# Optimization experiments

Measured on AMD Instinct MI355X. Metric: run time of the kernel, lower is better.

## Reference

```python
import jax, jax.numpy as jnp
import numpy as np

INSIZE = 512
OUTSIZE = 512
N_U = 64
N_V = 64
SIGMA_MIN = 0.1
SIGMA_MAX = 1.0
BATCH = 8192


def setup_inputs() -> dict:
    key = jax.random.key(0)
    kx, kp, ku, kv, kb = jax.random.split(key, 5)
    x = jax.random.normal(kx, (BATCH, INSIZE), dtype=jnp.float32)
    nsigma = min(INSIZE, OUTSIZE)
    p = 0.001 * jax.random.normal(kp, (nsigma,), dtype=jnp.float32)
    U = jnp.triu(jax.random.normal(ku, (INSIZE, INSIZE), dtype=jnp.float32))
    V = jnp.triu(jax.random.normal(kv, (OUTSIZE, OUTSIZE), dtype=jnp.float32))
    bound = 1.0 / float(np.sqrt(INSIZE))
    bias = jax.random.uniform(kb, (1, OUTSIZE), minval=-bound, maxval=bound, dtype=jnp.float32)
    return {"x": x, "p": p, "U": U, "V": V, "bias": bias}


def _house_chain(x, rows):
    # Sequentially apply Householder reflections. rows[i] has its leading
    # entries zeroed (upper-triangular structure), which makes the full-width
    # dot/outer-product exactly equal to torch's Hprod on the trailing slice
    # u[-k:] while leaving the leading columns of x untouched.
    def step(x, u):
        alpha = 2.0 * (x @ u) / jnp.dot(u, u)  # [B]
        return x - alpha[:, None] * u[None, :], None
    x, _ = jax.lax.scan(step, x, rows)
    return x


def _sigma_matrix(p, dtype):
    r = (SIGMA_MAX - SIGMA_MIN) / 2.0
    sigma_mean = SIGMA_MIN + r
    sigmas = 2.0 * r * (jax.nn.sigmoid(p) - 0.5) + sigma_mean  # [nsigma]
    nsigma = min(INSIZE, OUTSIZE)
    idx = jnp.arange(nsigma)
    return jnp.zeros((INSIZE, OUTSIZE), dtype=dtype).at[idx, idx].set(sigmas.astype(dtype))


def reference(x, p, U, V, bias):
    # Umultiply: i = 0 .. N_U-1, reflector U[i] with k = insize - i
    x = _house_chain(x, jnp.triu(U)[:N_U])
    # x @ Sigma (rectangular diagonal of constrained singular values)
    x = x @ _sigma_matrix(p, x.dtype)
    # Vmultiply: i = N_V-1 down to 0, reflector V[i] with k = outsize - i
    x = _house_chain(x, jnp.triu(V)[:N_V][::-1])
    return x + bias
```

## Files before the change

kernel.cpp:

```cpp
#include <hip/hip_runtime.h>
#include <hip/hip_bf16.h>
#include <math.h>


#define INSIZE 512
#define NREF 64
#define BATCH 8192

static constexpr int OFF_WT    = 0;
static constexpr int OFF_SIGMA = 131072;
static constexpr int OFF_BETAU = OFF_SIGMA + 512;
static constexpr int OFF_BETAV = OFF_BETAU + 64;
static constexpr int OFF_GU    = OFF_BETAV + 64;
static constexpr int OFF_GV    = OFF_GU + 4096;
static constexpr int OFF_C     = OFF_GV + 4096;

__device__ inline float sigma_of(float pv) {
    float s = 1.0f / (1.0f + expf(-pv));
    return 0.55f + 0.9f * (s - 0.5f);
}

__global__ __launch_bounds__(256) void k_prep(const float* __restrict__ U,
                                              const float* __restrict__ V,
                                              const float* __restrict__ p,
                                              float* __restrict__ ws) {
    int b = blockIdx.x, t = threadIdx.x;
    if (b == 192) {
        for (int c = t; c < INSIZE; c += 256)
            (ws + OFF_SIGMA)[c] = sigma_of(p[c]);
        return;
    }
    __shared__ float rowi[INSIZE];
    int w = t >> 6, l = t & 63;
    if (b < 128) {
        bool isV = (b >= 64);
        int i = isV ? (b - 64) : b;
        const float* src = isV ? V : U;
        int srow = isV ? (63 - i) : i;
        for (int c = t; c < INSIZE; c += 256) rowi[c] = src[srow * INSIZE + c];
        __syncthreads();
        float* G = ws + (isV ? OFF_GV : OFF_GU);
        float* beta = ws + (isV ? OFF_BETAV : OFF_BETAU);
        for (int jj = 0; jj < 16; ++jj) {
            int j = w * 16 + jj;
            int jrow = isV ? (63 - j) : j;
            const float* rj = src + jrow * INSIZE;
            float s = 0.f;
            for (int c = l; c < INSIZE; c += 64) s += rowi[c] * rj[c];
            for (int o = 32; o > 0; o >>= 1) s += __shfl_down(s, o, 64);
            if (l == 0) {
                G[i * 64 + j] = s;
                if (j == i) beta[i] = 2.0f / s;
            }
        }
    } else {
        int i = b - 128;
        for (int c = t; c < INSIZE; c += 256)
            rowi[c] = U[i * INSIZE + c] * sigma_of(p[c]);
        __syncthreads();
        float* C = ws + OFF_C;
        for (int jj = 0; jj < 16; ++jj) {
            int j = w * 16 + jj;
            const float* rj = V + (63 - j) * INSIZE;
            float s = 0.f;
            for (int c = l; c < INSIZE; c += 64) s += rowi[c] * rj[c];
            for (int o = 32; o > 0; o >>= 1) s += __shfl_down(s, o, 64);
            if (l == 0) C[i * 64 + j] = s;
        }
    }
}

__global__ __launch_bounds__(256) void k_WtE(const float* __restrict__ U,
                                             const float* __restrict__ V,
                                             float* __restrict__ ws) {
    __shared__ float Ps[128][34];
    __shared__ float Qs[128][34];
    __shared__ float Xs[4160];
    int t = threadIdx.x;
    int r0 = (blockIdx.x >> 4) * 32;
    int c0 = (blockIdx.x & 15) * 32;
    const float* sig = ws + OFF_SIGMA;
    float* Qf = &Qs[0][0];

    for (int i = t; i < 1024; i += 256) {
        *(float4*)&Xs[i * 4] = *(const float4*)&(ws + OFF_GU)[i * 4];
        *(float4*)&Qf[i * 4] = *(const float4*)&(ws + OFF_GV)[i * 4];
    }
    if (t < 64) {
        Xs[4096 + t] = (ws + OFF_BETAU)[t];
        Qf[4096 + t] = (ws + OFF_BETAV)[t];
    }
    __syncthreads();

    float partR[64];
    if (t < 32) {
        int r = r0 + t;
        float part[64];
#pragma unroll
        for (int j = 0; j < 64; ++j) part[j] = U[j * INSIZE + r];
#pragma unroll
        for (int m = 0; m < 64; ++m) {
            float am = part[m] * Xs[4096 + m];
            part[m] = am;
#pragma unroll
            for (int j = m + 1; j < 64; ++j)
                part[j] -= am * Xs[m * 64 + j];
        }
#pragma unroll
        for (int j = 0; j < 64; ++j) Ps[j][t] = part[j];
    } else if (t < 64) {
        int c = c0 + (t - 32);
#pragma unroll
        for (int i = 0; i < 64; ++i) partR[i] = V[(63 - i) * INSIZE + c];
#pragma unroll
        for (int i = 63; i >= 0; --i) {
            float s = partR[i];
#pragma unroll
            for (int m = i + 1; m < 64; ++m)
                s -= Qf[i * 64 + m] * partR[m];
            partR[i] = s * Qf[4096 + i];
        }
    }
    __syncthreads();

    for (int i = t; i < 1024; i += 256)
        *(float4*)&Xs[i * 4] = *(const float4*)&(ws + OFF_C)[i * 4];
    int lr = t & 31, kb = t >> 5;
    float sc = sig[c0 + lr];
#pragma unroll
    for (int ii = 0; ii < 8; ++ii) {
        int k = kb + ii * 8;
        Qs[k][lr] = U[k * INSIZE + c0 + lr] * sc;
    }
    if (t >= 32 && t < 64) {
#pragma unroll
        for (int i = 0; i < 64; ++i) Qs[64 + i][t - 32] = partR[i];
    }
    __syncthreads();

    float sr = sig[r0 + lr];
#pragma unroll
    for (int ii = 0; ii < 8; ++ii) {
        int j = kb * 8 + ii;
        float e = sr * V[(63 - j) * INSIZE + r0 + lr];
#pragma unroll 8
        for (int i = 0; i < 64; ++i)
            e -= Ps[i][lr] * Xs[i * 64 + j];
        Ps[64 + j][lr] = e;
    }
    __syncthreads();

    int ty = t >> 4, tx = t & 15;
    float a00 = 0.f, a01 = 0.f, a10 = 0.f, a11 = 0.f;
#pragma unroll
    for (int k = 0; k < 128; ++k) {
        float2 a = *(const float2*)&Ps[k][ty * 2];
        float2 bq = *(const float2*)&Qs[k][tx * 2];
        a00 += a.x * bq.x; a01 += a.x * bq.y;
        a10 += a.y * bq.x; a11 += a.y * bq.y;
    }
    int rg = r0 + ty * 2, cg = c0 + tx * 2;
    float w00 = ((rg == cg) ? sig[rg] : 0.f) - a00;
    float w01 = ((rg == cg + 1) ? sig[rg] : 0.f) - a01;
    float w10 = ((rg + 1 == cg) ? sig[rg + 1] : 0.f) - a10;
    float w11 = ((rg + 1 == cg + 1) ? sig[rg + 1] : 0.f) - a11;
    unsigned short* Wt = (unsigned short*)(ws + OFF_WT);
    __hip_bfloat162 lo = __float22bfloat162_rn(make_float2(w00, w10));
    __hip_bfloat162 hi = __float22bfloat162_rn(make_float2(w01, w11));
    *(__hip_bfloat162*)&Wt[cg * INSIZE + rg] = lo;
    *(__hip_bfloat162*)&Wt[(cg + 1) * INSIZE + rg] = hi;
}

typedef __attribute__((ext_vector_type(8))) short short8;
typedef __attribute__((ext_vector_type(4))) float float4v;

__global__ __launch_bounds__(256) void k_gemm(const float* __restrict__ X,
                                              const float* __restrict__ ws,
                                              const float* __restrict__ bias,
                                              float* __restrict__ out) {
    __shared__ float As[64 * 32];
    __shared__ unsigned short Bs[128 * 32];
    const unsigned short* Wt = (const unsigned short*)(ws + OFF_WT);

    int L = blockIdx.x;
    int inner = L & 7;
    int bn = (L >> 3) & 3;
    int bm = (L >> 5) * 8 + inner;
    int row0 = bm * 64, col0 = bn * 128;

    int t = threadIdx.x;
    int l = t & 63, w = t >> 6;
    int wm = (w & 1) * 32, wn = (w >> 1) * 64;

    float4v acc[2][4] = {};
    int quad = l >> 4;
    int lan = l & 15;

    for (int k0 = 0; k0 < INSIZE; k0 += 32) {
        __syncthreads();
#pragma unroll
        for (int i = 0; i < 2; ++i) {
            int P = i * 256 + t;
            int prow = P >> 3, pc = P & 7;
            int lc = pc ^ (prow & 7);
            const float* g = X + (size_t)(row0 + prow) * INSIZE + k0 + lc * 4;
            __builtin_amdgcn_global_load_lds(
                (const __attribute__((address_space(1))) void*)g,
                (__attribute__((address_space(3))) void*)(As + P * 4), 16, 0, 0);
        }
#pragma unroll
        for (int i = 0; i < 2; ++i) {
            int P = i * 256 + t;
            int prow = P >> 2, pc = P & 3;
            int lc = pc ^ ((prow >> 1) & 3);
            const unsigned short* g = Wt + (size_t)(col0 + prow) * INSIZE + k0 + lc * 8;
            __builtin_amdgcn_global_load_lds(
                (const __attribute__((address_space(1))) void*)g,
                (__attribute__((address_space(3))) void*)(Bs + P * 8), 16, 0, 0);
        }
        __syncthreads();

        short8 af[2];
        short8 bf[4];
#pragma unroll
        for (int mi = 0; mi < 2; ++mi) {
            int rl = wm + mi * 16 + lan;
            int c0q = quad * 2;
            const float4v lo = *(const float4v*)(As + (rl * 8 + (c0q ^ (rl & 7))) * 4);
            const float4v hi = *(const float4v*)(As + (rl * 8 + ((c0q + 1) ^ (rl & 7))) * 4);
            union { short8 s; __hip_bfloat162 h[4]; } u;
            u.h[0] = __float22bfloat162_rn(make_float2(lo[0], lo[1]));
            u.h[1] = __float22bfloat162_rn(make_float2(lo[2], lo[3]));
            u.h[2] = __float22bfloat162_rn(make_float2(hi[0], hi[1]));
            u.h[3] = __float22bfloat162_rn(make_float2(hi[2], hi[3]));
            af[mi] = u.s;
        }
#pragma unroll
        for (int ni = 0; ni < 4; ++ni) {
            int rn = wn + ni * 16 + lan;
            int c = quad ^ ((rn >> 1) & 3);
            bf[ni] = *(const short8*)(Bs + (rn * 4 + c) * 8);
        }
#pragma unroll
        for (int mi = 0; mi < 2; ++mi)
#pragma unroll
            for (int ni = 0; ni < 4; ++ni)
                acc[mi][ni] = __builtin_amdgcn_mfma_f32_16x16x32_bf16(
                    af[mi], bf[ni], acc[mi][ni], 0, 0, 0);
    }

#pragma unroll
    for (int ni = 0; ni < 4; ++ni) {
        int c = col0 + wn + ni * 16 + lan;
        float bv = bias[c];
#pragma unroll
        for (int mi = 0; mi < 2; ++mi) {
            int rbase = row0 + wm + mi * 16 + quad * 4;
#pragma unroll
            for (int r = 0; r < 4; ++r)
                out[(size_t)(rbase + r) * INSIZE + c] = acc[mi][ni][r] + bv;
        }
    }
}

extern "C" void kernel_launch(void* const* d_in, const int* in_sizes, int n_in,
                              void* d_out, int out_size, void* d_ws, size_t ws_size,
                              hipStream_t stream) {
    const float* x    = (const float*)d_in[0];
    const float* p    = (const float*)d_in[1];
    const float* U    = (const float*)d_in[2];
    const float* V    = (const float*)d_in[3];
    const float* bias = (const float*)d_in[4];
    float* ws  = (float*)d_ws;
    float* out = (float*)d_out;

    k_prep<<<193, 256, 0, stream>>>(U, V, p, ws);
    k_WtE<<<256, 256, 0, stream>>>(U, V, ws);
    k_gemm<<<512, 256, 0, stream>>>(x, ws, bias, out);
}
```

Measured before the change: 131.8 us.

## Parallelize triangular solves across full block and shrink GEMM column tile

The serial 64-step triangular solves in k_WtE, which previously ran on only 32 or 64 threads, are now spread over all 256 threads. Each lane holds 8 entries and broadcasts the pivot coefficient with a wavefront shuffle. The Gram matrices are masked to their strict triangle so the full-width update loops stay correct. The GEMM column tile also drops from 128 to 64 with twice as many blocks, raising occupancy at the cost of more redundant loading of X.

```diff
diff --git a/kernel.cpp b/kernel.cpp
--- a/kernel.cpp
+++ b/kernel.cpp
@@ -49,7 +49,8 @@
             for (int c = l; c < INSIZE; c += 64) s += rowi[c] * rj[c];
             for (int o = 32; o > 0; o >>= 1) s += __shfl_down(s, o, 64);
             if (l == 0) {
-                G[i * 64 + j] = s;
+                bool keep = isV ? (j < i) : (j > i);
+                G[i * 64 + j] = keep ? s : 0.0f;
                 if (j == i) beta[i] = 2.0f / s;
             }
         }
@@ -92,33 +93,40 @@
     }
     __syncthreads();
 
-    float partR[64];
-    if (t < 32) {
-        int r = r0 + t;
-        float part[64];
-#pragma unroll
-        for (int j = 0; j < 64; ++j) part[j] = U[j * INSIZE + r];
+    int l = t & 63;
+    int c_loc = (t >> 6) * 8 + (l >> 3);
+    int grp = l & 7;
+    int srcbase = l & 0x38;
+    float pj[8], pr[8];
+    {
+        int r = r0 + c_loc;
+#pragma unroll
+        for (int jj = 0; jj < 8; ++jj) pj[jj] = U[(grp * 8 + jj) * INSIZE + r];
 #pragma unroll
         for (int m = 0; m < 64; ++m) {
-            float am = part[m] * Xs[4096 + m];
-            part[m] = am;
-#pragma unroll
-            for (int j = m + 1; j < 64; ++j)
-                part[j] -= am * Xs[m * 64 + j];
-        }
-#pragma unroll
-        for (int j = 0; j < 64; ++j) Ps[j][t] = part[j];
-    } else if (t < 64) {
-        int c = c0 + (t - 32);
-#pragma unroll
-        for (int i = 0; i < 64; ++i) partR[i] = V[(63 - i) * INSIZE + c];
+            float tmp = pj[m & 7] * Xs[4096 + m];
+            float am = __shfl(tmp, srcbase | (m >> 3), 64);
+            if (grp == (m >> 3)) pj[m & 7] = am;
+#pragma unroll
+            for (int jj = 0; jj < 8; ++jj)
+                pj[jj] -= am * Xs[m * 64 + grp * 8 + jj];
+        }
+#pragma unroll
+        for (int jj = 0; jj < 8; ++jj) Ps[grp * 8 + jj][c_loc] = pj[jj];
+    }
+    {
+        int c = c0 + c_loc;
+#pragma unroll
+        for (int ii = 0; ii < 8; ++ii)
+            pr[ii] = V[(63 - (grp * 8 + ii)) * INSIZE + c];
 #pragma unroll
         for (int i = 63; i >= 0; --i) {
-            float s = partR[i];
-#pragma unroll
-            for (int m = i + 1; m < 64; ++m)
-                s -= Qf[i * 64 + m] * partR[m];
-            partR[i] = s * Qf[4096 + i];
+            float tmp = pr[i & 7] * Qf[4096 + i];
+            float ai = __shfl(tmp, srcbase | (i >> 3), 64);
+            if (grp == (i >> 3)) pr[i & 7] = ai;
+#pragma unroll
+            for (int ii = 0; ii < 8; ++ii)
+                pr[ii] -= ai * Qf[i * 64 + grp * 8 + ii];
         }
     }
     __syncthreads();
@@ -132,10 +140,9 @@
         int k = kb + ii * 8;
         Qs[k][lr] = U[k * INSIZE + c0 + lr] * sc;
     }
-    if (t >= 32 && t < 64) {
-#pragma unroll
-        for (int i = 0; i < 64; ++i) Qs[64 + i][t - 32] = partR[i];
-    }
+#pragma unroll
+    for (int ii = 0; ii < 8; ++ii)
+        Qs[64 + grp * 8 + ii][c_loc] = pr[ii];
     __syncthreads();
 
     float sr = sig[r0 + lr];
@@ -179,20 +186,20 @@
                                               const float* __restrict__ bias,
                                               float* __restrict__ out) {
     __shared__ float As[64 * 32];
-    __shared__ unsigned short Bs[128 * 32];
+    __shared__ unsigned short Bs[64 * 32];
     const unsigned short* Wt = (const unsigned short*)(ws + OFF_WT);
 
     int L = blockIdx.x;
     int inner = L & 7;
-    int bn = (L >> 3) & 3;
-    int bm = (L >> 5) * 8 + inner;
-    int row0 = bm * 64, col0 = bn * 128;
+    int bn = (L >> 3) & 7;
+    int bm = (L >> 6) * 8 + inner;
+    int row0 = bm * 64, col0 = bn * 64;
 
     int t = threadIdx.x;
     int l = t & 63, w = t >> 6;
-    int wm = (w & 1) * 32, wn = (w >> 1) * 64;
-
-    float4v acc[2][4] = {};
+    int wm = (w & 1) * 32, wn = (w >> 1) * 32;
+
+    float4v acc[2][2] = {};
     int quad = l >> 4;
     int lan = l & 15;
 
@@ -208,9 +215,8 @@
                 (const __attribute__((address_space(1))) void*)g,
                 (__attribute__((address_space(3))) void*)(As + P * 4), 16, 0, 0);
         }
-#pragma unroll
-        for (int i = 0; i < 2; ++i) {
-            int P = i * 256 + t;
+        {
+            int P = t;
             int prow = P >> 2, pc = P & 3;
             int lc = pc ^ ((prow >> 1) & 3);
             const unsigned short* g = Wt + (size_t)(col0 + prow) * INSIZE + k0 + lc * 8;
@@ -221,7 +227,7 @@
         __syncthreads();
 
         short8 af[2];
-        short8 bf[4];
+        short8 bf[2];
 #pragma unroll
         for (int mi = 0; mi < 2; ++mi) {
             int rl = wm + mi * 16 + lan;
@@ -236,7 +242,7 @@
             af[mi] = u.s;
         }
 #pragma unroll
-        for (int ni = 0; ni < 4; ++ni) {
+        for (int ni = 0; ni < 2; ++ni) {
             int rn = wn + ni * 16 + lan;
             int c = quad ^ ((rn >> 1) & 3);
             bf[ni] = *(const short8*)(Bs + (rn * 4 + c) * 8);
@@ -244,13 +250,13 @@
 #pragma unroll
         for (int mi = 0; mi < 2; ++mi)
 #pragma unroll
-            for (int ni = 0; ni < 4; ++ni)
+            for (int ni = 0; ni < 2; ++ni)
                 acc[mi][ni] = __builtin_amdgcn_mfma_f32_16x16x32_bf16(
                     af[mi], bf[ni], acc[mi][ni], 0, 0, 0);
     }
 
 #pragma unroll
-    for (int ni = 0; ni < 4; ++ni) {
+    for (int ni = 0; ni < 2; ++ni) {
         int c = col0 + wn + ni * 16 + lan;
         float bv = bias[c];
 #pragma unroll
@@ -276,5 +282,5 @@
 
     k_prep<<<193, 256, 0, stream>>>(U, V, p, ws);
     k_WtE<<<256, 256, 0, stream>>>(U, V, ws);
-    k_gemm<<<512, 256, 0, stream>>>(x, ws, bias, out);
-}
+    k_gemm<<<1024, 256, 0, stream>>>(x, ws, bias, out);
+}
```

Result: faster. 113.6 us (-13.8%).
